# Kernel tuning notes

Measured on AMD Instinct MI355X. Metric: run time of the kernel, lower is better.

## Reference

```python
import jax, jax.numpy as jnp
import numpy as np


def setup_inputs() -> dict:
    key = jax.random.key(0)
    k1, k2 = jax.random.split(key)
    shape = (128, 100, 6, 32, 32)
    output = jax.random.normal(k1, shape, dtype=jnp.float32)
    convdata = jax.random.normal(k2, shape, dtype=jnp.float32)
    return {"output": output, "convdata": convdata}


def reference(output, convdata):
    # Original: sum over 32x32 grid of mean(|convdata[:,:,0:3,i,j] - output[:,:,0:3,i,j]|) / 1024.
    # Each per-cell mean is over an identical-sized slice, so this equals the
    # global mean of |diff| over the [:, :, 0:3, :, :] region.
    diff = jnp.abs(convdata[:, :, 0:3, :, :] - output[:, :, 0:3, :, :])
    return jnp.mean(diff)
```

## Files before the change

### kernel.cpp

```cpp
#include <hip/hip_runtime.h>


#define NVEC      9830400
#define VEC_USED  768
#define VEC_PITCH 1536
#define NBLOCKS   2048
#define NTHREADS  256

__global__ __launch_bounds__(NTHREADS)
void abs_diff_partial(const float4* __restrict__ a4,
                      const float4* __restrict__ b4,
                      float* __restrict__ partials) {
    float sum = 0.0f;
    const int stride = gridDim.x * blockDim.x;
    for (int vid = blockIdx.x * blockDim.x + threadIdx.x; vid < NVEC; vid += stride) {
        int p = vid / VEC_USED;
        int r = vid - p * VEC_USED;
        int src = p * VEC_PITCH + r;
        float4 a = a4[src];
        float4 b = b4[src];
        sum += fabsf(b.x - a.x) + fabsf(b.y - a.y)
             + fabsf(b.z - a.z) + fabsf(b.w - a.w);
    }
    #pragma unroll
    for (int off = 32; off > 0; off >>= 1)
        sum += __shfl_down(sum, off, 64);
    __shared__ float lds[NTHREADS / 64];
    const int wave = threadIdx.x >> 6;
    const int lane = threadIdx.x & 63;
    if (lane == 0) lds[wave] = sum;
    __syncthreads();
    if (threadIdx.x == 0) {
        float s = 0.0f;
        #pragma unroll
        for (int w = 0; w < NTHREADS / 64; ++w) s += lds[w];
        partials[blockIdx.x] = s;
    }
}

__global__ __launch_bounds__(NTHREADS)
void final_reduce(const float* __restrict__ partials,
                  float* __restrict__ out) {
    float sum = 0.0f;
    for (int i = threadIdx.x; i < NBLOCKS; i += NTHREADS)
        sum += partials[i];
    #pragma unroll
    for (int off = 32; off > 0; off >>= 1)
        sum += __shfl_down(sum, off, 64);
    __shared__ float lds[NTHREADS / 64];
    const int wave = threadIdx.x >> 6;
    const int lane = threadIdx.x & 63;
    if (lane == 0) lds[wave] = sum;
    __syncthreads();
    if (threadIdx.x == 0) {
        float s = 0.0f;
        #pragma unroll
        for (int w = 0; w < NTHREADS / 64; ++w) s += lds[w];
        out[0] = s * (1.0f / 39321600.0f);
    }
}

extern "C" void kernel_launch(void* const* d_in, const int* in_sizes, int n_in,
                              void* d_out, int out_size, void* d_ws, size_t ws_size,
                              hipStream_t stream) {
    const float4* output4   = (const float4*)d_in[0];
    const float4* convdata4 = (const float4*)d_in[1];
    float* partials = (float*)d_ws;
    float* out = (float*)d_out;

    abs_diff_partial<<<NBLOCKS, NTHREADS, 0, stream>>>(output4, convdata4, partials);
    final_reduce<<<1, NTHREADS, 0, stream>>>(partials, out);
}
```

Baseline: 530.1 us.

## Map one block per (batch,channel) slab with unrolled loads, widen final reduce

Replaces the grid-stride loop, with its per-element divide and modulo address math, by one block per 128x100 slab. Each thread issues three independent float4 loads from each input, giving more memory-level parallelism and no index arithmetic. This raises the partial count to 12800, so the final reduction runs with 1024 threads to absorb the larger tail. The trade-off is many short-lived blocks with launch overhead and a heavier single-block final pass.

```diff
diff --git a/kernel.cpp b/kernel.cpp
--- a/kernel.cpp
+++ b/kernel.cpp
@@ -1,30 +1,35 @@
 #include <hip/hip_runtime.h>
 
 
-#define NVEC      9830400
+#define NPAIRS    12800
 #define VEC_USED  768
 #define VEC_PITCH 1536
-#define NBLOCKS   2048
 #define NTHREADS  256
 
 __global__ __launch_bounds__(NTHREADS)
 void abs_diff_partial(const float4* __restrict__ a4,
                       const float4* __restrict__ b4,
                       float* __restrict__ partials) {
-    float sum = 0.0f;
-    const int stride = gridDim.x * blockDim.x;
-    for (int vid = blockIdx.x * blockDim.x + threadIdx.x; vid < NVEC; vid += stride) {
-        int p = vid / VEC_USED;
-        int r = vid - p * VEC_USED;
-        int src = p * VEC_PITCH + r;
-        float4 a = a4[src];
-        float4 b = b4[src];
-        sum += fabsf(b.x - a.x) + fabsf(b.y - a.y)
-             + fabsf(b.z - a.z) + fabsf(b.w - a.w);
-    }
+    const size_t base = (size_t)blockIdx.x * VEC_PITCH + threadIdx.x;
+
+    float4 a0 = a4[base];
+    float4 b0 = b4[base];
+    float4 a1 = a4[base + NTHREADS];
+    float4 b1 = b4[base + NTHREADS];
+    float4 a2 = a4[base + 2 * NTHREADS];
+    float4 b2 = b4[base + 2 * NTHREADS];
+
+    float sum = fabsf(b0.x - a0.x) + fabsf(b0.y - a0.y)
+              + fabsf(b0.z - a0.z) + fabsf(b0.w - a0.w)
+              + fabsf(b1.x - a1.x) + fabsf(b1.y - a1.y)
+              + fabsf(b1.z - a1.z) + fabsf(b1.w - a1.w)
+              + fabsf(b2.x - a2.x) + fabsf(b2.y - a2.y)
+              + fabsf(b2.z - a2.z) + fabsf(b2.w - a2.w);
+
     #pragma unroll
     for (int off = 32; off > 0; off >>= 1)
         sum += __shfl_down(sum, off, 64);
+
     __shared__ float lds[NTHREADS / 64];
     const int wave = threadIdx.x >> 6;
     const int lane = threadIdx.x & 63;
@@ -38,16 +43,17 @@
     }
 }
 
-__global__ __launch_bounds__(NTHREADS)
+#define FTHREADS 1024
+__global__ __launch_bounds__(FTHREADS)
 void final_reduce(const float* __restrict__ partials,
                   float* __restrict__ out) {
     float sum = 0.0f;
-    for (int i = threadIdx.x; i < NBLOCKS; i += NTHREADS)
+    for (int i = threadIdx.x; i < NPAIRS; i += FTHREADS)
         sum += partials[i];
     #pragma unroll
     for (int off = 32; off > 0; off >>= 1)
         sum += __shfl_down(sum, off, 64);
-    __shared__ float lds[NTHREADS / 64];
+    __shared__ float lds[FTHREADS / 64];
     const int wave = threadIdx.x >> 6;
     const int lane = threadIdx.x & 63;
     if (lane == 0) lds[wave] = sum;
@@ -55,7 +61,7 @@
     if (threadIdx.x == 0) {
         float s = 0.0f;
         #pragma unroll
-        for (int w = 0; w < NTHREADS / 64; ++w) s += lds[w];
+        for (int w = 0; w < FTHREADS / 64; ++w) s += lds[w];
         out[0] = s * (1.0f / 39321600.0f);
     }
 }
@@ -68,6 +74,6 @@
     float* partials = (float*)d_ws;
     float* out = (float*)d_out;
 
-    abs_diff_partial<<<NBLOCKS, NTHREADS, 0, stream>>>(output4, convdata4, partials);
-    final_reduce<<<1, NTHREADS, 0, stream>>>(partials, out);
+    abs_diff_partial<<<NPAIRS, NTHREADS, 0, stream>>>(output4, convdata4, partials);
+    final_reduce<<<1, FTHREADS, 0, stream>>>(partials, out);
 }
```

Result: no change. 526.4 us (-0.7%).
